# Performance work log

Measured on AMD Instinct MI355X. Metric: run time of the kernel, lower is better.

The kernel has to match this reference:

```python
import jax, jax.numpy as jnp
import numpy as np

T, B, H = 2048, 8, 1024


def setup_inputs() -> dict:
    key = jax.random.key(0)
    ks = jax.random.split(key, 4)
    scale = 1.0 / np.sqrt(H)
    x = jax.random.normal(ks[0], (T, B, H), dtype=jnp.float32)
    W_q = jax.random.normal(ks[1], (H, H), dtype=jnp.float32) * scale
    b_q = jnp.zeros((H,), dtype=jnp.float32)
    beta_raw = jax.random.normal(ks[2], (H,), dtype=jnp.float32)
    W_fc = jax.random.normal(ks[3], (H, H), dtype=jnp.float32) * scale
    b_fc = jnp.zeros((H,), dtype=jnp.float32)
    return {"x": x, "W_q": W_q, "b_q": b_q, "beta_raw": beta_raw,
            "W_fc": W_fc, "b_fc": b_fc}


def reference(x, W_q, b_q, beta_raw, W_fc, b_fc):
    # Per-neuron learned leak in (0,1)
    beta = jax.nn.sigmoid(beta_raw)  # (H,)
    # Input (q) projection: (T,B,H) @ (H,H)^T
    q = jnp.einsum('tbh,oh->tbo', x, W_q) + b_q  # (T,B,H)
    # Leaky integration m_t = beta * m_{t-1} + q_t as an associative scan over T
    a = jnp.broadcast_to(beta, q.shape)  # (T,B,H)

    def combine(c1, c2):
        a1, m1 = c1
        a2, m2 = c2
        return (a1 * a2, a2 * m1 + m2)

    _, m = jax.lax.associative_scan(combine, (a, q), axis=0)  # (T,B,H)
    # Linear + ReLU
    h = jnp.einsum('tbh,oh->tbo', m, W_fc) + b_fc
    return jax.nn.relu(h)
```

## Files before the change

### kernel.cpp

```cpp
#include <hip/hip_runtime.h>
#include <stdint.h>

typedef unsigned short u16;
typedef __bf16 bf16x8 __attribute__((ext_vector_type(8)));
typedef float f32x4 __attribute__((ext_vector_type(4)));

__device__ __forceinline__ u16 f2bf(float f) {
  union { float f; uint32_t u; } x; x.f = f;
  uint32_t u = x.u;
  u += 0x7fffu + ((u >> 16) & 1u);
  return (u16)(u >> 16);
}
__device__ __forceinline__ float bf2f(uint32_t lo16) {
  union { uint32_t u; float f; } x; x.u = lo16 << 16; return x.f;
}
__device__ __forceinline__ float bfhi(uint32_t u) {
  union { uint32_t u; float f; } x; x.u = u & 0xffff0000u; return x.f;
}
__device__ __forceinline__ uint32_t fixpair(uint32_t m, float p0, float p1,
                                            float F0, float F1) {
  float e0 = fmaf(p0, F0, bf2f(m & 0xffffu));
  float e1 = fmaf(p1, F1, bfhi(m));
  return (uint32_t)f2bf(e0) | ((uint32_t)f2bf(e1) << 16);
}

__device__ __forceinline__ void async_load16(const u16* g, u16* l) {
  __builtin_amdgcn_global_load_lds(
      (const __attribute__((address_space(1))) void*)g,
      (__attribute__((address_space(3))) void*)l,
      16, 0, 0);
}

__global__ __launch_bounds__(256) void prep_all(const float* __restrict__ x,
                                                const float* __restrict__ Wq,
                                                const float* __restrict__ Wfc,
                                                const float* __restrict__ braw,
                                                u16* __restrict__ xb,
                                                u16* __restrict__ wqb,
                                                u16* __restrict__ wfcb,
                                                float* __restrict__ beta,
                                                float* __restrict__ bpow) {
  int gid = blockIdx.x * 256 + threadIdx.x;
  if (gid < 1024) {
    float b = 1.0f / (1.0f + expf(-braw[gid]));
    beta[gid] = b;
    float w = b;
#pragma unroll 1
    for (int p = 1; p <= 32; p++) { bpow[p * 1024 + gid] = w; w *= b; }
  }
  if (gid < 131072) {
    const int HH = 1024 * 1024;
    int i = gid * 16;
    const float* src = (i < HH) ? (Wq + i) : (Wfc + (i - HH));
    u16* dst = (i < HH) ? (wqb + i) : (wfcb + (i - HH));
#pragma unroll
    for (int c = 0; c < 4; c++) {
      float4 v = *(const float4*)(src + c * 4);
      ushort4 o = {f2bf(v.x), f2bf(v.y), f2bf(v.z), f2bf(v.w)};
      *(ushort4*)(dst + c * 4) = o;
    }
  }
  {
    int i = gid * 8;
    float4 a = *(const float4*)(x + i);
    float4 b = *(const float4*)(x + i + 4);
    ushort4 o0 = {f2bf(a.x), f2bf(a.y), f2bf(a.z), f2bf(a.w)};
    ushort4 o1 = {f2bf(b.x), f2bf(b.y), f2bf(b.z), f2bf(b.w)};
    *(ushort4*)(xb + i) = o0;
    *(ushort4*)(xb + i + 4) = o1;
  }
}

__global__ __launch_bounds__(512, 2) void gemm_scan(const u16* __restrict__ A,
                                                    const u16* __restrict__ B,
                                                    const float* __restrict__ bias,
                                                    u16* __restrict__ Cout,
                                                    const float* __restrict__ beta_arr,
                                                    float* __restrict__ carry_out,
                                                    int M, int N, int K) {
  __shared__ u16 lds[4][2][256 * 32];

  const int tid  = threadIdx.x;
  const int lane = tid & 63;
  const int wid  = tid >> 6;
  const int wr   = (wid >> 2) * 128;
  const int wc   = (wid & 3) * 64;

  const int bid    = blockIdx.x;
  const int xcd    = bid & 7;
  const int idx    = bid >> 3;
  const int tile_m = ((xcd << 3) | (idx >> 2)) * 256;
  const int tile_n = (idx & 3) * 256;

  const int srow    = tid >> 2;
  const int schunk  = (tid & 3) ^ ((srow >> 1) & 3);
  const u16* gA = A + (size_t)(tile_m + srow) * K + schunk * 8;
  const u16* gB = B + (size_t)(tile_n + srow) * K + schunk * 8;
  const size_t half_stride = (size_t)128 * K;

#define STAGE(slot, kt)                                                   \
  do {                                                                    \
    const size_t k0 = (size_t)(kt) * 32;                                  \
    async_load16(gA + k0,               &lds[slot][0][wid * 512]);        \
    async_load16(gA + k0 + half_stride, &lds[slot][0][4096 + wid * 512]); \
    async_load16(gB + k0,               &lds[slot][1][wid * 512]);        \
    async_load16(gB + k0 + half_stride, &lds[slot][1][4096 + wid * 512]); \
  } while (0)

  f32x4 acc[8][4];
#pragma unroll
  for (int i = 0; i < 8; i++)
#pragma unroll
    for (int j = 0; j < 4; j++) acc[i][j] = (f32x4){0.f, 0.f, 0.f, 0.f};

  const int lrow = lane & 15;
  const int kq   = lane >> 4;
  const int kc   = (lrow >> 1) & 3;
  const int coff = ((kq ^ kc) << 3);

  const int NKT = K >> 5;

  STAGE(0, 0);
  if (NKT > 1) STAGE(1, 1);
  if (NKT > 2) STAGE(2, 2);
  if (NKT > 2)      asm volatile("s_waitcnt vmcnt(8)" ::: "memory");
  else if (NKT > 1) asm volatile("s_waitcnt vmcnt(4)" ::: "memory");
  else              asm volatile("s_waitcnt vmcnt(0)" ::: "memory");
  __builtin_amdgcn_s_barrier();

  for (int kt = 0; kt < NKT; ++kt) {
    const int slot = kt & 3;
    const u16* As = &lds[slot][0][0];
    const u16* Bs = &lds[slot][1][0];

    bf16x8 a[8], b[4];
#pragma unroll
    for (int i = 0; i < 8; i++)
      a[i] = *(const bf16x8*)&As[(wr + i * 16 + lrow) * 32 + coff];
#pragma unroll
    for (int j = 0; j < 4; j++)
      b[j] = *(const bf16x8*)&Bs[(wc + j * 16 + lrow) * 32 + coff];

    if (kt + 3 < NKT) STAGE((kt + 3) & 3, kt + 3);

    __builtin_amdgcn_s_setprio(1);
#pragma unroll
    for (int i = 0; i < 8; i++)
#pragma unroll
      for (int j = 0; j < 4; j++)
        acc[i][j] = __builtin_amdgcn_mfma_f32_16x16x32_bf16(a[i], b[j], acc[i][j], 0, 0, 0);
    __builtin_amdgcn_s_setprio(0);

    const int ahead = NKT - 1 - kt;
    if (ahead >= 3) {
      asm volatile("s_waitcnt vmcnt(8)" ::: "memory");
      __builtin_amdgcn_s_barrier();
    } else if (ahead == 2) {
      asm volatile("s_waitcnt vmcnt(4)" ::: "memory");
      __builtin_amdgcn_s_barrier();
    } else if (ahead == 1) {
      asm volatile("s_waitcnt vmcnt(0)" ::: "memory");
      __builtin_amdgcn_s_barrier();
    }
  }
#undef STAGE

  const int crow = (lane >> 4) << 2;
  const int ccol = lane & 15;
  const int c4   = lane >> 4;
  const int kap  = c4 >> 1;
  const int Wh   = wr >> 7;
  float* sm15 = (float*)&lds[0][0][0];

#pragma unroll
  for (int j = 0; j < 4; j++) {
    const int gn = tile_n + wc + j * 16 + ccol;
    const float bv = bias[gn];
    const float be = beta_arr[gn];
    const float be2 = be * be;
#pragma unroll
    for (int r = 0; r < 4; r++) {
      float S[8], R[8];
      S[0] = acc[0][j][r] + bv;
#pragma unroll
      for (int i = 1; i < 8; i++) S[i] = fmaf(be2, S[i - 1], acc[i][j][r] + bv);
#pragma unroll
      for (int i = 0; i < 8; i++) R[i] = __shfl_xor(S[i], 32);
      acc[0][j][r] = kap ? fmaf(be, R[0], S[0]) : S[0];
#pragma unroll
      for (int i = 1; i < 8; i++)
        acc[i][j][r] = fmaf(be, kap ? R[i] : R[i - 1], S[i]);
    }
  }
  if (Wh == 0 && kap == 1) {
#pragma unroll
    for (int j = 0; j < 4; j++)
#pragma unroll
      for (int r = 0; r < 4; r++) {
        const int bb = ((c4 << 2) + r) & 7;
        sm15[bb * 256 + wc + j * 16 + ccol] = acc[7][j][r];
      }
  }
  __syncthreads();
  if (Wh == 1) {
#pragma unroll
    for (int j = 0; j < 4; j++) {
      const int hl = wc + j * 16 + ccol;
      const float be = beta_arr[tile_n + hl];
      const float be2 = be * be;
#pragma unroll
      for (int r = 0; r < 4; r++) {
        const int bb = ((c4 << 2) + r) & 7;
        const float v = sm15[bb * 256 + hl];
        float f = kap ? be2 : be;
#pragma unroll
        for (int i = 0; i < 8; i++) {
          acc[i][j][r] = fmaf(f, v, acc[i][j][r]);
          f *= be2;
        }
      }
    }
  }
#pragma unroll
  for (int i = 0; i < 8; i++) {
#pragma unroll
    for (int j = 0; j < 4; j++) {
      const int gm = tile_m + wr + i * 16 + crow;
      const int gn = tile_n + wc + j * 16 + ccol;
#pragma unroll
      for (int r = 0; r < 4; r++)
        Cout[(size_t)(gm + r) * N + gn] = f2bf(acc[i][j][r]);
    }
  }
  if (Wh == 1 && kap == 1) {
    const int seg = tile_m >> 8;
#pragma unroll
    for (int j = 0; j < 4; j++) {
      const int hl = wc + j * 16 + ccol;
#pragma unroll
      for (int r = 0; r < 4; r++) {
        const int bb = ((c4 << 2) + r) & 7;
        carry_out[(size_t)seg * 8192 + bb * 1024 + tile_n + hl] = acc[7][j][r];
      }
    }
  }
}

__global__ __launch_bounds__(256) void ffold(const float4* __restrict__ carry4,
                                             const float* __restrict__ bpow,
                                             float4* __restrict__ Fbuf) {
  const int cq = blockIdx.x * 256 + threadIdx.x;
  const int hq = cq & 255;
  const float4 b32 = *(const float4*)&bpow[32 * 1024 + hq * 4];
  float4 F = make_float4(0.f, 0.f, 0.f, 0.f);
  for (int s = 0; s < 64; s++) {
    Fbuf[(size_t)s * 2048 + cq] = F;
    float4 c = carry4[(size_t)s * 2048 + cq];
    F.x = fmaf(b32.x, F.x, c.x);
    F.y = fmaf(b32.y, F.y, c.y);
    F.z = fmaf(b32.z, F.z, c.z);
    F.w = fmaf(b32.w, F.w, c.w);
  }
}

__global__ __launch_bounds__(256) void mfix(const uint4* __restrict__ mloc,
                                            const float* __restrict__ bpow,
                                            const float* __restrict__ Fbuf,
                                            uint4* __restrict__ mout) {
  const int stride = gridDim.x * 256;
  const int total  = 16384 * 128;
  for (int idx = blockIdx.x * 256 + threadIdx.x; idx < total; idx += stride) {
    const int r   = idx >> 7;
    const int hq  = idx & 127;
    const int seg = r >> 8;
    const int rl  = r & 255;
    const int tl  = rl >> 3;
    const int b   = rl & 7;
    const float* p = bpow + (size_t)(tl + 1) * 1024 + hq * 8;
    const float* f = Fbuf + (size_t)seg * 8192 + b * 1024 + hq * 8;
    const float4 p0 = *(const float4*)p,       p1 = *(const float4*)(p + 4);
    const float4 f0 = *(const float4*)f,       f1 = *(const float4*)(f + 4);
    const uint4 m = mloc[idx];
    uint4 o;
    o.x = fixpair(m.x, p0.x, p0.y, f0.x, f0.y);
    o.y = fixpair(m.y, p0.z, p0.w, f0.z, f0.w);
    o.z = fixpair(m.z, p1.x, p1.y, f1.x, f1.y);
    o.w = fixpair(m.w, p1.z, p1.w, f1.z, f1.w);
    mout[idx] = o;
  }
}

__global__ __launch_bounds__(512, 2) void gemm_relu(const u16* __restrict__ A,
                                                    const u16* __restrict__ B,
                                                    const float* __restrict__ bias,
                                                    float* __restrict__ Cout,
                                                    int M, int N, int K) {
  __shared__ u16 lds[4][2][256 * 32];

  const int tid  = threadIdx.x;
  const int lane = tid & 63;
  const int wid  = tid >> 6;
  const int wr   = (wid >> 2) * 128;
  const int wc   = (wid & 3) * 64;

  const int bid    = blockIdx.x;
  const int xcd    = bid & 7;
  const int idx    = bid >> 3;
  const int tile_m = ((xcd << 3) | (idx >> 2)) * 256;
  const int tile_n = (idx & 3) * 256;

  const int srow    = tid >> 2;
  const int schunk  = (tid & 3) ^ ((srow >> 1) & 3);
  const u16* gA = A + (size_t)(tile_m + srow) * K + schunk * 8;
  const u16* gB = B + (size_t)(tile_n + srow) * K + schunk * 8;
  const size_t half_stride = (size_t)128 * K;

#define STAGE(slot, kt)                                                   \
  do {                                                                    \
    const size_t k0 = (size_t)(kt) * 32;                                  \
    async_load16(gA + k0,               &lds[slot][0][wid * 512]);        \
    async_load16(gA + k0 + half_stride, &lds[slot][0][4096 + wid * 512]); \
    async_load16(gB + k0,               &lds[slot][1][wid * 512]);        \
    async_load16(gB + k0 + half_stride, &lds[slot][1][4096 + wid * 512]); \
  } while (0)

  f32x4 acc[8][4];
#pragma unroll
  for (int i = 0; i < 8; i++)
#pragma unroll
    for (int j = 0; j < 4; j++) acc[i][j] = (f32x4){0.f, 0.f, 0.f, 0.f};

  const int lrow = lane & 15;
  const int kq   = lane >> 4;
  const int kc   = (lrow >> 1) & 3;
  const int coff = ((kq ^ kc) << 3);

  const int NKT = K >> 5;

  STAGE(0, 0);
  if (NKT > 1) STAGE(1, 1);
  if (NKT > 2) STAGE(2, 2);
  if (NKT > 2)      asm volatile("s_waitcnt vmcnt(8)" ::: "memory");
  else if (NKT > 1) asm volatile("s_waitcnt vmcnt(4)" ::: "memory");
  else              asm volatile("s_waitcnt vmcnt(0)" ::: "memory");
  __builtin_amdgcn_s_barrier();

  for (int kt = 0; kt < NKT; ++kt) {
    const int slot = kt & 3;
    const u16* As = &lds[slot][0][0];
    const u16* Bs = &lds[slot][1][0];

    bf16x8 a[8], b[4];
#pragma unroll
    for (int i = 0; i < 8; i++)
      a[i] = *(const bf16x8*)&As[(wr + i * 16 + lrow) * 32 + coff];
#pragma unroll
    for (int j = 0; j < 4; j++)
      b[j] = *(const bf16x8*)&Bs[(wc + j * 16 + lrow) * 32 + coff];

    if (kt + 3 < NKT) STAGE((kt + 3) & 3, kt + 3);

    __builtin_amdgcn_s_setprio(1);
#pragma unroll
    for (int i = 0; i < 8; i++)
#pragma unroll
      for (int j = 0; j < 4; j++)
        acc[i][j] = __builtin_amdgcn_mfma_f32_16x16x32_bf16(a[i], b[j], acc[i][j], 0, 0, 0);
    __builtin_amdgcn_s_setprio(0);

    const int ahead = NKT - 1 - kt;
    if (ahead >= 3) {
      asm volatile("s_waitcnt vmcnt(8)" ::: "memory");
      __builtin_amdgcn_s_barrier();
    } else if (ahead == 2) {
      asm volatile("s_waitcnt vmcnt(4)" ::: "memory");
      __builtin_amdgcn_s_barrier();
    } else if (ahead == 1) {
      asm volatile("s_waitcnt vmcnt(0)" ::: "memory");
      __builtin_amdgcn_s_barrier();
    }
  }
#undef STAGE

  const int crow = (lane >> 4) << 2;
  const int ccol = lane & 15;
#pragma unroll
  for (int i = 0; i < 8; i++) {
#pragma unroll
    for (int j = 0; j < 4; j++) {
      const int gm = tile_m + wr + i * 16 + crow;
      const int gn = tile_n + wc + j * 16 + ccol;
      const float bv = bias[gn];
#pragma unroll
      for (int r = 0; r < 4; r++) {
        float v = acc[i][j][r] + bv;
        v = fmaxf(v, 0.f);
        Cout[(size_t)(gm + r) * N + gn] = v;
      }
    }
  }
}

extern "C" void kernel_launch(void* const* d_in, const int* in_sizes, int n_in,
                              void* d_out, int out_size, void* d_ws, size_t ws_size,
                              hipStream_t stream) {
  const float* x        = (const float*)d_in[0];
  const float* W_q      = (const float*)d_in[1];
  const float* b_q      = (const float*)d_in[2];
  const float* beta_raw = (const float*)d_in[3];
  const float* W_fc     = (const float*)d_in[4];
  const float* b_fc     = (const float*)d_in[5];

  const int H = 1024;
  const int M = 2048 * 8;
  const size_t MH = (size_t)M * H;

  char* ws = (char*)d_ws;
  u16* x_bf    = (u16*)ws;  ws += MH * 2;
  u16* m_loc   = (u16*)ws;  ws += MH * 2;
  u16* m_fix   = (u16*)ws;  ws += MH * 2;
  u16* wq_bf   = (u16*)ws;  ws += (size_t)H * H * 2;
  u16* wfc_bf  = (u16*)ws;  ws += (size_t)H * H * 2;
  float* beta  = (float*)ws; ws += 4096;
  float* bpow  = (float*)ws; ws += 33 * 1024 * 4;
  float* carry = (float*)ws; ws += (size_t)64 * 8192 * 4;
  float* Fbuf  = (float*)ws; ws += (size_t)64 * 8192 * 4;

  prep_all<<<(int)(MH / 8 / 256), 256, 0, stream>>>(x, W_q, W_fc, beta_raw,
                                                    x_bf, wq_bf, wfc_bf, beta, bpow);

  gemm_scan<<<256, 512, 0, stream>>>(x_bf, wq_bf, b_q, m_loc, beta, carry, M, H, H);

  ffold<<<8, 256, 0, stream>>>((const float4*)carry, bpow, (float4*)Fbuf);

  mfix<<<2048, 256, 0, stream>>>((const uint4*)m_loc, bpow, Fbuf, (uint4*)m_fix);

  gemm_relu<<<256, 512, 0, stream>>>(m_fix, wfc_bf, b_fc, (float*)d_out, M, H, H);
}
```

Measured before the change: 240.8 us.

## Fuse carry fold into fixup kernel with per-block redundant prefix

Replaces the serial ffold kernel and the mfix kernel with one scanfix kernel. Each block recomputes the carry prefix for its own segment and 32-column slice into shared memory, then applies the fixup to its 256 rows. This removes a launch and the low-parallelism serial fold plus the Fbuf round trip through memory. In exchange it adds redundant carry reads, load imbalance across segments, and a less coalesced row-strided access pattern in the fixup.

```diff
diff --git a/kernel.cpp b/kernel.cpp
--- a/kernel.cpp
+++ b/kernel.cpp
@@ -246,47 +246,53 @@
   }
 }
 
-__global__ __launch_bounds__(256) void ffold(const float4* __restrict__ carry4,
-                                             const float* __restrict__ bpow,
-                                             float4* __restrict__ Fbuf) {
-  const int cq = blockIdx.x * 256 + threadIdx.x;
-  const int hq = cq & 255;
-  const float4 b32 = *(const float4*)&bpow[32 * 1024 + hq * 4];
-  float4 F = make_float4(0.f, 0.f, 0.f, 0.f);
-  for (int s = 0; s < 64; s++) {
-    Fbuf[(size_t)s * 2048 + cq] = F;
-    float4 c = carry4[(size_t)s * 2048 + cq];
-    F.x = fmaf(b32.x, F.x, c.x);
-    F.y = fmaf(b32.y, F.y, c.y);
-    F.z = fmaf(b32.z, F.z, c.z);
-    F.w = fmaf(b32.w, F.w, c.w);
-  }
-}
-
-__global__ __launch_bounds__(256) void mfix(const uint4* __restrict__ mloc,
-                                            const float* __restrict__ bpow,
-                                            const float* __restrict__ Fbuf,
-                                            uint4* __restrict__ mout) {
-  const int stride = gridDim.x * 256;
-  const int total  = 16384 * 128;
-  for (int idx = blockIdx.x * 256 + threadIdx.x; idx < total; idx += stride) {
-    const int r   = idx >> 7;
-    const int hq  = idx & 127;
-    const int seg = r >> 8;
-    const int rl  = r & 255;
-    const int tl  = rl >> 3;
-    const int b   = rl & 7;
-    const float* p = bpow + (size_t)(tl + 1) * 1024 + hq * 8;
-    const float* f = Fbuf + (size_t)seg * 8192 + b * 1024 + hq * 8;
-    const float4 p0 = *(const float4*)p,       p1 = *(const float4*)(p + 4);
-    const float4 f0 = *(const float4*)f,       f1 = *(const float4*)(f + 4);
-    const uint4 m = mloc[idx];
-    uint4 o;
-    o.x = fixpair(m.x, p0.x, p0.y, f0.x, f0.y);
-    o.y = fixpair(m.y, p0.z, p0.w, f0.z, f0.w);
-    o.z = fixpair(m.z, p1.x, p1.y, f1.x, f1.y);
-    o.w = fixpair(m.w, p1.z, p1.w, f1.z, f1.w);
-    mout[idx] = o;
+__global__ __launch_bounds__(256) void scanfix(const u16* __restrict__ mloc,
+                                               const float* __restrict__ carry,
+                                               const float* __restrict__ bpow,
+                                               u16* __restrict__ mout) {
+  __shared__ float F_lds[8 * 33];
+
+  const int tid  = threadIdx.x;
+  const int seg  = blockIdx.x >> 5;
+  const int part = blockIdx.x & 31;
+  const int h0   = part * 32;
+
+  {
+    const int fb = tid >> 5;
+    const int hh = tid & 31;
+    const int h  = h0 + hh;
+    const float w = bpow[32 * 1024 + h];
+    float F = 0.f;
+    const float* cp = carry + fb * 1024 + h;
+#pragma unroll 4
+    for (int s = 0; s < seg; s++) F = fmaf(w, F, cp[(size_t)s * 8192]);
+    F_lds[fb * 33 + hh] = F;
+  }
+  __syncthreads();
+
+  {
+    const int rl = tid;
+    const int tl = rl >> 3;
+    const int b  = rl & 7;
+    const size_t row = (size_t)(seg * 256 + rl) * 1024 + h0;
+    const uint4* mi = (const uint4*)(mloc + row);
+    uint4*       mo = (uint4*)(mout + row);
+    const float* p  = bpow + (size_t)(tl + 1) * 1024 + h0;
+    const float* Fp = &F_lds[b * 33];
+#pragma unroll
+    for (int q = 0; q < 4; q++) {
+      const uint4 m = mi[q];
+      const float4 p0 = *(const float4*)(p + q * 8);
+      const float4 p1 = *(const float4*)(p + q * 8 + 4);
+      const float4 f0 = *(const float4*)(Fp + q * 8);
+      const float4 f1 = *(const float4*)(Fp + q * 8 + 4);
+      uint4 o;
+      o.x = fixpair(m.x, p0.x, p0.y, f0.x, f0.y);
+      o.y = fixpair(m.y, p0.z, p0.w, f0.z, f0.w);
+      o.z = fixpair(m.z, p1.x, p1.y, f1.x, f1.y);
+      o.w = fixpair(m.w, p1.z, p1.w, f1.z, f1.w);
+      mo[q] = o;
+    }
   }
 }
 
@@ -424,16 +430,13 @@
   float* beta  = (float*)ws; ws += 4096;
   float* bpow  = (float*)ws; ws += 33 * 1024 * 4;
   float* carry = (float*)ws; ws += (size_t)64 * 8192 * 4;
-  float* Fbuf  = (float*)ws; ws += (size_t)64 * 8192 * 4;
 
   prep_all<<<(int)(MH / 8 / 256), 256, 0, stream>>>(x, W_q, W_fc, beta_raw,
                                                     x_bf, wq_bf, wfc_bf, beta, bpow);
 
   gemm_scan<<<256, 512, 0, stream>>>(x_bf, wq_bf, b_q, m_loc, beta, carry, M, H, H);
 
-  ffold<<<8, 256, 0, stream>>>((const float4*)carry, bpow, (float4*)Fbuf);
-
-  mfix<<<2048, 256, 0, stream>>>((const uint4*)m_loc, bpow, Fbuf, (uint4*)m_fix);
+  scanfix<<<2048, 256, 0, stream>>>(m_loc, carry, bpow, m_fix);
 
   gemm_relu<<<256, 512, 0, stream>>>(m_fix, wfc_bf, b_fc, (float*)d_out, M, H, H);
 }
```

After: 250.0 us. +3.8%, slower.
